# Performance work log

Measured on AMD Instinct MI355X. Metric: run time of the kernel, lower is better.

The kernel has to match this reference:

```python
import jax, jax.numpy as jnp
import numpy as np

V_IN = 32000   # input vocab
V_OUT = 32000  # output vocab
H = 512        # hidden size
T = 128        # encoder max length
B = 64         # batch
MAXLEN = 32    # decoder steps
BOS = 2


def gru_cell(x, h, Wih, Whh, bih, bhh):
    # PyTorch GRU gate order: r, z, n
    gi = x @ Wih.T + bih          # (B, 3H)
    gh = h @ Whh.T + bhh          # (B, 3H)
    i_r, i_z, i_n = jnp.split(gi, 3, axis=-1)
    h_r, h_z, h_n = jnp.split(gh, 3, axis=-1)
    r = jax.nn.sigmoid(i_r + h_r)
    z = jax.nn.sigmoid(i_z + h_z)
    n = jnp.tanh(i_n + r * h_n)
    return (1.0 - z) * n + z * h


def setup_inputs() -> dict:
    key = jax.random.key(0)
    ks = jax.random.split(key, 14)
    s = 1.0 / np.sqrt(H)

    def U(k, shape):
        return jax.random.uniform(k, shape, jnp.float32, -s, s)

    tok = jax.random.randint(ks[0], (T, B), 1, V_IN)
    lengths_X = jax.random.randint(ks[1], (B,), 1, T + 1)
    valid = jnp.arange(T)[:, None] < lengths_X[None, :]
    batch_X = jnp.where(valid, tok, 0)  # PAD=0 beyond length

    return {
        "batch_X": batch_X,
        "lengths_X": lengths_X,
        "max_length": MAXLEN,
        "emb_enc": U(ks[2], (V_IN, H)).at[0].set(0.0),   # padding_idx=0
        "Wih_e": U(ks[3], (3 * H, H)),
        "Whh_e": U(ks[4], (3 * H, H)),
        "bih_e": U(ks[5], (3 * H,)),
        "bhh_e": U(ks[6], (3 * H,)),
        "emb_dec": U(ks[7], (V_OUT, H)).at[0].set(0.0),  # padding_idx=0
        "Wih_d": U(ks[8], (3 * H, H)),
        "Whh_d": U(ks[9], (3 * H, H)),
        "bih_d": U(ks[10], (3 * H,)),
        "bhh_d": U(ks[11], (3 * H,)),
        "Wout": U(ks[12], (V_OUT, H)),
        "bout": U(ks[13], (V_OUT,)),
    }


def reference(batch_X, lengths_X, max_length,
              emb_enc, Wih_e, Whh_e, bih_e, bhh_e,
              emb_dec, Wih_d, Whh_d, bih_d, bhh_d,
              Wout, bout):
    t_len, bsz = batch_X.shape
    emb = emb_enc[batch_X]                               # (T, B, H)
    mask = jnp.arange(t_len)[:, None] < lengths_X[None, :]  # (T, B)

    def enc_step(h, inp):
        x, m = inp
        h_new = gru_cell(x, h, Wih_e, Whh_e, bih_e, bhh_e)
        # packed-sequence semantics: hidden freezes after each seq's length
        return jnp.where(m[:, None], h_new, h), None

    h0 = jnp.zeros((bsz, emb_enc.shape[1]), emb.dtype)
    h_enc, _ = jax.lax.scan(enc_step, h0, (emb, mask))

    def dec_step(carry, _):
        tok, h = carry
        e = emb_dec[tok]                                 # (B, H)
        h = gru_cell(e, h, Wih_d, Whh_d, bih_d, bhh_d)
        logits = h @ Wout.T + bout                       # (B, V_OUT)
        return (jnp.argmax(logits, axis=-1), h), logits

    init = (jnp.full((bsz,), BOS, dtype=batch_X.dtype), h_enc)
    _, outputs = jax.lax.scan(dec_step, init, None, length=max_length)
    return outputs  # (max_length, B, V_OUT)
```

## Files before the change

### kernel.cpp

```cpp
#include <hip/hip_runtime.h>
#include <math.h>

constexpr int NB  = 64;
constexpr int NH  = 512;
constexpr int BOSTOK = 2;

__device__ __forceinline__ float sigmoidf_(float x) { return 1.0f / (1.0f + expf(-x)); }

__global__ __launch_bounds__(256) void k_init(float* __restrict__ eT,
                                              const float* __restrict__ emb_dec) {
    int i = blockIdx.x * 256 + threadIdx.x;
    if (i < NH * NB) eT[i] = emb_dec[BOSTOK * NH + (i >> 6)];
}

__global__ __launch_bounds__(256) void k_xg(const int* __restrict__ tokens,
                                            const float* __restrict__ emb,
                                            float* __restrict__ xg, int total_f4) {
    int idx = blockIdx.x * 256 + threadIdx.x;
    int stride = gridDim.x * 256;
    for (int f = idx; f < total_f4; f += stride) {
        const int tb = f >> 7;
        const int kq = f & 127;
        const int row = tokens[tb];
        ((float4*)xg)[f] = ((const float4*)(emb + (size_t)row * NH))[kq];
    }
}

__global__ __launch_bounds__(256) void k_wpack(const float* __restrict__ Whh,
                                               float4* __restrict__ Wp) {
    const int gk = blockIdx.x;
    const int g = gk >> 7, kq = gk & 127;
    for (int j = threadIdx.x; j < NH; j += 256) {
        const float* src = Whh + ((size_t)(g * NH + j)) * NH + 4 * kq;
        Wp[(size_t)gk * NH + j] = make_float4(src[0], src[1], src[2], src[3]);
    }
}

__global__ __launch_bounds__(256) void k_gi(const float* __restrict__ xg,
                                            const float* __restrict__ Wih,
                                            float* __restrict__ gi) {
    __shared__ __align__(16) float At[2][16][68];
    __shared__ __align__(16) float Bs[2][16][132];
    const int tid  = threadIdx.x;
    const int tb0  = blockIdx.y * 64;
    const int gj0  = blockIdx.x * 128;
    const int g_tb = tid >> 4;
    const int g_gj = tid & 15;
    const int a_tb = tid >> 2, a_kq = tid & 3;
    const int b_gj = tid >> 2, b_kq = tid & 3;

    float4 ra, rb0, rb1;
    ra  = *(const float4*)(xg  + (size_t)(tb0 + a_tb) * NH + 4 * a_kq);
    rb0 = *(const float4*)(Wih + (size_t)(gj0 + b_gj) * NH + 4 * b_kq);
    rb1 = *(const float4*)(Wih + (size_t)(gj0 + b_gj + 64) * NH + 4 * b_kq);

    float acc[4][8];
#pragma unroll
    for (int a = 0; a < 4; ++a)
#pragma unroll
        for (int b = 0; b < 8; ++b) acc[a][b] = 0.f;

    for (int c = 0; c < NH / 16; ++c) {
        const int buf = c & 1;
#pragma unroll
        for (int q = 0; q < 4; ++q) {
            At[buf][4 * a_kq + q][a_tb]      = ((const float*)&ra)[q];
            Bs[buf][4 * b_kq + q][b_gj]      = ((const float*)&rb0)[q];
            Bs[buf][4 * b_kq + q][b_gj + 64] = ((const float*)&rb1)[q];
        }
        __syncthreads();
        if (c + 1 < NH / 16) {
            const int k0 = (c + 1) * 16;
            ra  = *(const float4*)(xg  + (size_t)(tb0 + a_tb) * NH + k0 + 4 * a_kq);
            rb0 = *(const float4*)(Wih + (size_t)(gj0 + b_gj) * NH + k0 + 4 * b_kq);
            rb1 = *(const float4*)(Wih + (size_t)(gj0 + b_gj + 64) * NH + k0 + 4 * b_kq);
        }
#pragma unroll
        for (int k = 0; k < 16; ++k) {
            const float4 av = *(const float4*)&At[buf][k][4 * g_tb];
            const float4 b0 = *(const float4*)&Bs[buf][k][8 * g_gj];
            const float4 b1 = *(const float4*)&Bs[buf][k][8 * g_gj + 4];
            const float* ap  = (const float*)&av;
            const float* bp0 = (const float*)&b0;
            const float* bp1 = (const float*)&b1;
#pragma unroll
            for (int a = 0; a < 4; ++a) {
#pragma unroll
                for (int b = 0; b < 4; ++b) {
                    acc[a][b]     += ap[a] * bp0[b];
                    acc[a][b + 4] += ap[a] * bp1[b];
                }
            }
        }
    }
    float* go = gi + (size_t)tb0 * (3 * NH) + gj0;
#pragma unroll
    for (int a = 0; a < 4; ++a) {
        float4 s0 = make_float4(acc[a][0], acc[a][1], acc[a][2], acc[a][3]);
        float4 s1 = make_float4(acc[a][4], acc[a][5], acc[a][6], acc[a][7]);
        float* r = go + (size_t)(4 * g_tb + a) * (3 * NH) + 8 * g_gj;
        *(float4*)(r)     = s0;
        *(float4*)(r + 4) = s1;
    }
}

__global__ __launch_bounds__(512, 1) void k_enc_recur(
        const float* __restrict__ gi,
        const float4* __restrict__ Wp,
        const float* __restrict__ bih, const float* __restrict__ bhh,
        const int* __restrict__ lengths,
        float* __restrict__ hfin) {
    __shared__ __align__(16) float hbuf[2][NH];
    const int b = blockIdx.x;
    const int j = threadIdx.x;
    const int len = lengths[b];
    const float bir  = bih[j],          bhr = bhh[j];
    const float biz  = bih[NH + j],     bhz = bhh[NH + j];
    const float bin_ = bih[2 * NH + j], bhn = bhh[2 * NH + j];
    hbuf[0][j] = 0.f;
    __syncthreads();
    int cur = 0;
    for (int t = 0; t < len; ++t) {
        const float* __restrict__ hs = hbuf[cur];
        const float* __restrict__ gp = gi + ((size_t)t * NB + b) * (3 * NH);
        float ar = 0.f, az = 0.f, an = 0.f;
#pragma unroll 4
        for (int kq = 0; kq < NH / 4; ++kq) {
            const float4 hq = *(const float4*)&hs[4 * kq];
            const float4 wr = Wp[(size_t)(0 * 128 + kq) * NH + j];
            const float4 wz = Wp[(size_t)(1 * 128 + kq) * NH + j];
            const float4 wn = Wp[(size_t)(2 * 128 + kq) * NH + j];
            ar += wr.x * hq.x + wr.y * hq.y + wr.z * hq.z + wr.w * hq.w;
            az += wz.x * hq.x + wz.y * hq.y + wz.z * hq.z + wz.w * hq.w;
            an += wn.x * hq.x + wn.y * hq.y + wn.z * hq.z + wn.w * hq.w;
        }
        const float r = sigmoidf_(gp[j] + bir + ar + bhr);
        const float z = sigmoidf_(gp[NH + j] + biz + az + bhz);
        const float n = tanhf(gp[2 * NH + j] + bin_ + r * (an + bhn));
        const float hv = (1.f - z) * n + z * hs[j];
        hbuf[cur ^ 1][j] = hv;
        __syncthreads();
        cur ^= 1;
    }
    hfin[(size_t)j * NB + b] = hbuf[cur][j];
}

__global__ __launch_bounds__(256) void k_dec_gru(const float* __restrict__ hc,
                                                 float* __restrict__ hn,
                                                 const float* __restrict__ eT,
                                                 const float* __restrict__ Wih,
                                                 const float* __restrict__ Whh,
                                                 const float* __restrict__ bih,
                                                 const float* __restrict__ bhh) {
    const int tid = threadIdx.x;
    const int b = tid & 63;
    const int jj = tid >> 6;
    const int j = blockIdx.x * 4 + jj;
    const float* __restrict__ ir_w = Wih + (size_t)j * NH;
    const float* __restrict__ iz_w = Wih + (size_t)(NH + j) * NH;
    const float* __restrict__ in_w = Wih + (size_t)(2 * NH + j) * NH;
    const float* __restrict__ hr_w = Whh + (size_t)j * NH;
    const float* __restrict__ hz_w = Whh + (size_t)(NH + j) * NH;
    const float* __restrict__ hn_w = Whh + (size_t)(2 * NH + j) * NH;
    float air = 0.f, aiz = 0.f, ain = 0.f;
    float ahr = 0.f, ahz = 0.f, ahn = 0.f;
#pragma unroll 2
    for (int k = 0; k < NH; k += 4) {
        const float4 a4 = *(const float4*)(ir_w + k);
        const float4 b4 = *(const float4*)(iz_w + k);
        const float4 c4 = *(const float4*)(in_w + k);
        const float4 d4 = *(const float4*)(hr_w + k);
        const float4 e4 = *(const float4*)(hz_w + k);
        const float4 f4 = *(const float4*)(hn_w + k);
        const float e0 = eT[(k + 0) * NB + b];
        const float e1 = eT[(k + 1) * NB + b];
        const float e2 = eT[(k + 2) * NB + b];
        const float e3 = eT[(k + 3) * NB + b];
        const float h0 = hc[(k + 0) * NB + b];
        const float h1 = hc[(k + 1) * NB + b];
        const float h2 = hc[(k + 2) * NB + b];
        const float h3 = hc[(k + 3) * NB + b];
        air += a4.x * e0 + a4.y * e1 + a4.z * e2 + a4.w * e3;
        aiz += b4.x * e0 + b4.y * e1 + b4.z * e2 + b4.w * e3;
        ain += c4.x * e0 + c4.y * e1 + c4.z * e2 + c4.w * e3;
        ahr += d4.x * h0 + d4.y * h1 + d4.z * h2 + d4.w * h3;
        ahz += e4.x * h0 + e4.y * h1 + e4.z * h2 + e4.w * h3;
        ahn += f4.x * h0 + f4.y * h1 + f4.z * h2 + f4.w * h3;
    }
    const float hj = hc[j * NB + b];
    const float r = sigmoidf_(air + bih[j] + ahr + bhh[j]);
    const float z = sigmoidf_(aiz + bih[NH + j] + ahz + bhh[NH + j]);
    const float n = tanhf(ain + bih[2 * NH + j] + r * (ahn + bhh[2 * NH + j]));
    const float hv = (1.f - z) * n + z * hj;
    hn[j * NB + b] = hv;
}

__global__ __launch_bounds__(256) void k_logits(const float* __restrict__ hT,
                                                const float* __restrict__ Wout,
                                                const float* __restrict__ bout,
                                                float* __restrict__ outp, int V) {
    __shared__ __align__(16) float Ws[2][32][128];
    __shared__ __align__(16) float Hs[2][32][64];
    const int tid = threadIdx.x;
    const int v0 = blockIdx.x * 128;
    const int vg = tid & 31;
    const int bg = tid >> 5;
    const int w_vl = tid >> 3;
    const int w_kq = tid & 7;

    float4 rw[4], rh[2];
#pragma unroll
    for (int p = 0; p < 4; ++p)
        rw[p] = *(const float4*)(Wout + (size_t)(v0 + w_vl + 32 * p) * NH + 4 * w_kq);
#pragma unroll
    for (int p = 0; p < 2; ++p)
        rh[p] = ((const float4*)hT)[p * 256 + tid];

    float acc[8][4];
#pragma unroll
    for (int i = 0; i < 8; ++i)
#pragma unroll
        for (int jv = 0; jv < 4; ++jv) acc[i][jv] = 0.f;

    for (int c = 0; c < 16; ++c) {
        const int buf = c & 1;
#pragma unroll
        for (int p = 0; p < 4; ++p)
#pragma unroll
            for (int q = 0; q < 4; ++q)
                Ws[buf][4 * w_kq + q][w_vl + 32 * p] = ((const float*)&rw[p])[q];
#pragma unroll
        for (int p = 0; p < 2; ++p)
            ((float4*)Hs[buf])[p * 256 + tid] = rh[p];
        __syncthreads();
        if (c + 1 < 16) {
            const int k0 = (c + 1) * 32;
#pragma unroll
            for (int p = 0; p < 4; ++p)
                rw[p] = *(const float4*)(Wout + (size_t)(v0 + w_vl + 32 * p) * NH + k0 + 4 * w_kq);
#pragma unroll
            for (int p = 0; p < 2; ++p)
                rh[p] = ((const float4*)(hT + (size_t)k0 * NB))[p * 256 + tid];
        }
#pragma unroll
        for (int k = 0; k < 32; ++k) {
            const float4 w  = *(const float4*)&Ws[buf][k][4 * vg];
            const float4 h0 = *(const float4*)&Hs[buf][k][8 * bg];
            const float4 h1 = *(const float4*)&Hs[buf][k][8 * bg + 4];
            const float* hp0 = (const float*)&h0;
            const float* hp1 = (const float*)&h1;
#pragma unroll
            for (int i = 0; i < 4; ++i) {
                acc[i][0] += hp0[i] * w.x; acc[i][1] += hp0[i] * w.y;
                acc[i][2] += hp0[i] * w.z; acc[i][3] += hp0[i] * w.w;
                acc[i + 4][0] += hp1[i] * w.x; acc[i + 4][1] += hp1[i] * w.y;
                acc[i + 4][2] += hp1[i] * w.z; acc[i + 4][3] += hp1[i] * w.w;
            }
        }
    }
    const float4 bo = *(const float4*)(bout + v0 + 4 * vg);
#pragma unroll
    for (int i = 0; i < 8; ++i) {
        float4 s = make_float4(acc[i][0] + bo.x, acc[i][1] + bo.y,
                               acc[i][2] + bo.z, acc[i][3] + bo.w);
        *(float4*)(outp + (size_t)(8 * bg + i) * V + v0 + 4 * vg) = s;
    }
}

__global__ __launch_bounds__(256) void k_argmax_embed(const float* __restrict__ logits_t,
                                                      const float* __restrict__ emb_dec,
                                                      float* __restrict__ eT,
                                                      int V) {
    const int b = blockIdx.x;
    const int tid = threadIdx.x;
    const float* __restrict__ lp = logits_t + (size_t)b * V;
    float best = -INFINITY;
    int bi = 0x7fffffff;
    for (int v = tid; v < V; v += 256) {
        const float x = lp[v];
        if (x > best) { best = x; bi = v; }
    }
    __shared__ float sv[256];
    __shared__ int si[256];
    sv[tid] = best;
    si[tid] = bi;
    __syncthreads();
    for (int s = 128; s > 0; s >>= 1) {
        if (tid < s) {
            const float ov = sv[tid + s];
            const int oi = si[tid + s];
            if (ov > sv[tid] || (ov == sv[tid] && oi < si[tid])) { sv[tid] = ov; si[tid] = oi; }
        }
        __syncthreads();
    }
    const int tok = si[0];
    const float* __restrict__ er = emb_dec + (size_t)tok * NH;
    for (int k = tid; k < NH; k += 256)
        eT[k * NB + b] = er[k];
}

extern "C" void kernel_launch(void* const* d_in, const int* in_sizes, int n_in,
                              void* d_out, int out_size, void* d_ws, size_t ws_size,
                              hipStream_t stream) {
    const int*   batch_X = (const int*)d_in[0];
    const int*   lengths = (const int*)d_in[1];
    const float* emb_enc = (const float*)d_in[3];
    const float* Wih_e   = (const float*)d_in[4];
    const float* Whh_e   = (const float*)d_in[5];
    const float* bih_e   = (const float*)d_in[6];
    const float* bhh_e   = (const float*)d_in[7];
    const float* emb_dec = (const float*)d_in[8];
    const float* Wih_d   = (const float*)d_in[9];
    const float* Whh_d   = (const float*)d_in[10];
    const float* bih_d   = (const float*)d_in[11];
    const float* bhh_d   = (const float*)d_in[12];
    const float* Wout    = (const float*)d_in[13];
    const float* bout    = (const float*)d_in[14];

    const int T = in_sizes[0] / NB;
    const int V = in_sizes[14];
    const int STEPS = out_size / (NB * V);

    float* out = (float*)d_out;

    float* dh0 = (float*)d_ws;
    float* dh1 = dh0 + NH * NB;
    float* eT  = dh1 + NH * NB;

    const size_t xg_off = (size_t)out_size - (size_t)T * NB * NH;
    const size_t gi_off = xg_off - (size_t)T * NB * 3 * NH;
    const size_t wp_off = gi_off - (size_t)3 * NH * NH;
    const size_t hf_off = wp_off - (size_t)NH * NB;
    float*  xg   = out + xg_off;
    float*  gi   = out + gi_off;
    float4* Wp   = (float4*)(out + wp_off);
    float*  hfin = out + hf_off;

    k_init<<<dim3(NH * NB / 256), dim3(256), 0, stream>>>(eT, emb_dec);
    k_xg<<<dim3(1024), dim3(256), 0, stream>>>(batch_X, emb_enc, xg, T * NB * NH / 4);
    k_wpack<<<dim3(3 * NH / 4), dim3(256), 0, stream>>>(Whh_e, Wp);
    k_gi<<<dim3(3 * NH / 128, T), dim3(256), 0, stream>>>(xg, Wih_e, gi);
    k_enc_recur<<<dim3(NB), dim3(512), 0, stream>>>(gi, Wp, bih_e, bhh_e, lengths, hfin);

    const float* hc = hfin;
    for (int s = 0; s < STEPS; ++s) {
        float* hn = (s & 1) ? dh1 : dh0;
        k_dec_gru<<<dim3(NH / 4), dim3(256), 0, stream>>>(
            hc, hn, eT, Wih_d, Whh_d, bih_d, bhh_d);
        float* out_t = out + (size_t)s * NB * V;
        k_logits<<<dim3(V / 128), dim3(256), 0, stream>>>(hn, Wout, bout, out_t, V);
        if (s + 1 < STEPS)
            k_argmax_embed<<<dim3(NB), dim3(256), 0, stream>>>(out_t, emb_dec, eT, V);
        hc = hn;
    }
}
```

Before: 7.372 ms.

## Split encoder GRU recurrence across 128 blocks with register-resident weights and atomic barriers

The encoder recurrence used to run one block per batch row, and each block streamed the whole packed Whh matrix from memory at every timestep. Now 128 blocks each own 32 hidden units for 8 batch rows. Each block keeps its Whh slice in registers, reduces partial dot products across lanes with DPP row sums, and exchanges hidden state through global memory. Steps are synchronised with per-batch-group atomic counters, which removes the Whh repack kernel and the repeated weight traffic but adds a cross-block spin barrier each step and relies on relaxed atomics for ordering. A minor readfirstlane hint is also added in the decoder GRU kernel.

```diff
diff --git a/kernel.cpp b/kernel.cpp
--- a/kernel.cpp
+++ b/kernel.cpp
@@ -4,13 +4,26 @@
 constexpr int NB  = 64;
 constexpr int NH  = 512;
 constexpr int BOSTOK = 2;
+constexpr int JT = 16;
+constexpr int BT = 8;
 
 __device__ __forceinline__ float sigmoidf_(float x) { return 1.0f / (1.0f + expf(-x)); }
 
+__device__ __forceinline__ float rowsum16(float v) {
+    int x;
+    x = __builtin_amdgcn_mov_dpp(__float_as_int(v), 0x128, 0xf, 0xf, false); v += __int_as_float(x);
+    x = __builtin_amdgcn_mov_dpp(__float_as_int(v), 0x124, 0xf, 0xf, false); v += __int_as_float(x);
+    x = __builtin_amdgcn_mov_dpp(__float_as_int(v), 0x122, 0xf, 0xf, false); v += __int_as_float(x);
+    x = __builtin_amdgcn_mov_dpp(__float_as_int(v), 0x121, 0xf, 0xf, false); v += __int_as_float(x);
+    return v;
+}
+
 __global__ __launch_bounds__(256) void k_init(float* __restrict__ eT,
-                                              const float* __restrict__ emb_dec) {
+                                              const float* __restrict__ emb_dec,
+                                              int* __restrict__ bar) {
     int i = blockIdx.x * 256 + threadIdx.x;
     if (i < NH * NB) eT[i] = emb_dec[BOSTOK * NH + (i >> 6)];
+    if (i < BT) __hip_atomic_store(&bar[i], 0, __ATOMIC_RELAXED, __HIP_MEMORY_SCOPE_AGENT);
 }
 
 __global__ __launch_bounds__(256) void k_xg(const int* __restrict__ tokens,
@@ -23,16 +36,6 @@
         const int kq = f & 127;
         const int row = tokens[tb];
         ((float4*)xg)[f] = ((const float4*)(emb + (size_t)row * NH))[kq];
-    }
-}
-
-__global__ __launch_bounds__(256) void k_wpack(const float* __restrict__ Whh,
-                                               float4* __restrict__ Wp) {
-    const int gk = blockIdx.x;
-    const int g = gk >> 7, kq = gk & 127;
-    for (int j = threadIdx.x; j < NH; j += 256) {
-        const float* src = Whh + ((size_t)(g * NH + j)) * NH + 4 * kq;
-        Wp[(size_t)gk * NH + j] = make_float4(src[0], src[1], src[2], src[3]);
     }
 }
 
@@ -104,45 +107,127 @@
     }
 }
 
-__global__ __launch_bounds__(512, 1) void k_enc_recur(
+__global__ __launch_bounds__(256, 1) void k_enc_recur(
         const float* __restrict__ gi,
-        const float4* __restrict__ Wp,
+        const float* __restrict__ Whh,
         const float* __restrict__ bih, const float* __restrict__ bhh,
         const int* __restrict__ lengths,
-        float* __restrict__ hfin) {
-    __shared__ __align__(16) float hbuf[2][NH];
-    const int b = blockIdx.x;
-    const int j = threadIdx.x;
-    const int len = lengths[b];
-    const float bir  = bih[j],          bhr = bhh[j];
-    const float biz  = bih[NH + j],     bhz = bhh[NH + j];
-    const float bin_ = bih[2 * NH + j], bhn = bhh[2 * NH + j];
-    hbuf[0][j] = 0.f;
-    __syncthreads();
-    int cur = 0;
-    for (int t = 0; t < len; ++t) {
-        const float* __restrict__ hs = hbuf[cur];
-        const float* __restrict__ gp = gi + ((size_t)t * NB + b) * (3 * NH);
-        float ar = 0.f, az = 0.f, an = 0.f;
-#pragma unroll 4
-        for (int kq = 0; kq < NH / 4; ++kq) {
-            const float4 hq = *(const float4*)&hs[4 * kq];
-            const float4 wr = Wp[(size_t)(0 * 128 + kq) * NH + j];
-            const float4 wz = Wp[(size_t)(1 * 128 + kq) * NH + j];
-            const float4 wn = Wp[(size_t)(2 * 128 + kq) * NH + j];
-            ar += wr.x * hq.x + wr.y * hq.y + wr.z * hq.z + wr.w * hq.w;
-            az += wz.x * hq.x + wz.y * hq.y + wz.z * hq.z + wz.w * hq.w;
-            an += wn.x * hq.x + wn.y * hq.y + wn.z * hq.z + wn.w * hq.w;
-        }
-        const float r = sigmoidf_(gp[j] + bir + ar + bhr);
-        const float z = sigmoidf_(gp[NH + j] + biz + az + bhz);
-        const float n = tanhf(gp[2 * NH + j] + bin_ + r * (an + bhn));
-        const float hv = (1.f - z) * n + z * hs[j];
-        hbuf[cur ^ 1][j] = hv;
-        __syncthreads();
-        cur ^= 1;
-    }
-    hfin[(size_t)j * NB + b] = hbuf[cur][j];
+        float* __restrict__ hx,
+        int* __restrict__ bar,
+        float* __restrict__ hfin,
+        int T) {
+    __shared__ __align__(16) float4 hsh[8 * 128];
+    const int tid = threadIdx.x;
+    const int jt = blockIdx.x >> 3;
+    const int bt = blockIdx.x & 7;
+    const int j0 = jt * 32;
+    const int b0 = bt * 8;
+    const int jg = tid >> 4;
+    const int ks = tid & 15;
+    const int k0 = ks * 32;
+
+    const int jo = j0 + jg * 2 + (ks >> 3);
+    const int bo = b0 + (ks & 7);
+
+    float4 wv[6][8];
+#pragma unroll
+    for (int jl = 0; jl < 2; ++jl)
+#pragma unroll
+        for (int g = 0; g < 3; ++g) {
+            const float* wr = Whh + ((size_t)(g * NH + j0 + jg * 2 + jl)) * NH + k0;
+#pragma unroll
+            for (int q = 0; q < 8; ++q)
+                wv[jl * 3 + g][q] = *(const float4*)(wr + 4 * q);
+        }
+
+    const float bir = bih[jo], biz = bih[NH + jo], bin_ = bih[2 * NH + jo];
+    const float bhr = bhh[jo], bhz = bhh[NH + jo], bhn  = bhh[2 * NH + jo];
+    const int   len = lengths[bo];
+    const float* __restrict__ gpr = gi + (size_t)bo * (3 * NH) + jo;
+    float hlast = 0.f;
+
+    for (int t = 0; t < T; ++t) {
+        if (t > 0 && tid == 0) {
+            const int tgt = JT * t;
+            while (__hip_atomic_load(&bar[bt], __ATOMIC_RELAXED, __HIP_MEMORY_SCOPE_AGENT) < tgt)
+                __builtin_amdgcn_s_sleep(1);
+        }
+        __syncthreads();
+
+        if (t == 0) {
+#pragma unroll
+            for (int i = 0; i < 4; ++i)
+                hsh[tid + i * 256] = make_float4(0.f, 0.f, 0.f, 0.f);
+        } else {
+            float4 v[4];
+#pragma unroll
+            for (int i = 0; i < 4; ++i) {
+                const int P = tid + i * 256;
+                const int bl = P >> 7, p = P & 127;
+                const int q = p ^ ((p >> 3) & 7);
+                float* src = hx + (size_t)(b0 + bl) * NH + q * 4;
+                v[i].x = __hip_atomic_load(src + 0, __ATOMIC_RELAXED, __HIP_MEMORY_SCOPE_AGENT);
+                v[i].y = __hip_atomic_load(src + 1, __ATOMIC_RELAXED, __HIP_MEMORY_SCOPE_AGENT);
+                v[i].z = __hip_atomic_load(src + 2, __ATOMIC_RELAXED, __HIP_MEMORY_SCOPE_AGENT);
+                v[i].w = __hip_atomic_load(src + 3, __ATOMIC_RELAXED, __HIP_MEMORY_SCOPE_AGENT);
+            }
+#pragma unroll
+            for (int i = 0; i < 4; ++i) {
+                const int P = tid + i * 256;
+                hsh[(P >> 7) * 128 + (P & 127)] = v[i];
+            }
+        }
+        __syncthreads();
+
+        float sr = 0.f, sz = 0.f, sn = 0.f;
+#pragma unroll
+        for (int b = 0; b < 8; ++b) {
+            float4 hq[8];
+#pragma unroll
+            for (int kk = 0; kk < 8; ++kk) {
+                const int q = ks * 8 + kk;
+                hq[kk] = hsh[b * 128 + (q ^ (ks & 7))];
+            }
+            float pr0 = 0.f, pz0 = 0.f, pn0 = 0.f, pr1 = 0.f, pz1 = 0.f, pn1 = 0.f;
+#pragma unroll
+            for (int kk = 0; kk < 8; ++kk) {
+                const float4 h4 = hq[kk];
+                const float4 w0 = wv[0][kk], w1 = wv[1][kk], w2 = wv[2][kk];
+                const float4 w3 = wv[3][kk], w4 = wv[4][kk], w5 = wv[5][kk];
+                pr0 += w0.x * h4.x + w0.y * h4.y + w0.z * h4.z + w0.w * h4.w;
+                pz0 += w1.x * h4.x + w1.y * h4.y + w1.z * h4.z + w1.w * h4.w;
+                pn0 += w2.x * h4.x + w2.y * h4.y + w2.z * h4.z + w2.w * h4.w;
+                pr1 += w3.x * h4.x + w3.y * h4.y + w3.z * h4.z + w3.w * h4.w;
+                pz1 += w4.x * h4.x + w4.y * h4.y + w4.z * h4.z + w4.w * h4.w;
+                pn1 += w5.x * h4.x + w5.y * h4.y + w5.z * h4.z + w5.w * h4.w;
+            }
+            pr0 = rowsum16(pr0); pz0 = rowsum16(pz0); pn0 = rowsum16(pn0);
+            pr1 = rowsum16(pr1); pz1 = rowsum16(pz1); pn1 = rowsum16(pn1);
+            if ((ks & 7) == b) {
+                if (ks >> 3) { sr = pr1; sz = pz1; sn = pn1; }
+                else         { sr = pr0; sz = pz0; sn = pn0; }
+            }
+        }
+
+        const float* __restrict__ gp = gpr + (size_t)t * NB * (3 * NH);
+        const float gr = gp[0], gz = gp[NH], gn = gp[2 * NH];
+        const int qj = jo >> 2;
+        const int pj = qj ^ ((qj >> 3) & 7);
+        const float hold = ((const float*)&hsh[(ks & 7) * 128 + pj])[jo & 3];
+        const float r = sigmoidf_(gr + bir + sr + bhr);
+        const float z = sigmoidf_(gz + biz + sz + bhz);
+        const float n = tanhf(gn + bin_ + r * (sn + bhn));
+        const float hv = (1.f - z) * n + z * hold;
+        if (t < len) {
+            __hip_atomic_store(hx + (size_t)bo * NH + jo, hv,
+                               __ATOMIC_RELAXED, __HIP_MEMORY_SCOPE_AGENT);
+            hlast = hv;
+        }
+        __syncthreads();
+        if (tid == 0)
+            __hip_atomic_fetch_add(&bar[bt], 1, __ATOMIC_RELAXED, __HIP_MEMORY_SCOPE_AGENT);
+    }
+    hfin[(size_t)jo * NB + bo] = hlast;
 }
 
 __global__ __launch_bounds__(256) void k_dec_gru(const float* __restrict__ hc,
@@ -154,7 +239,7 @@
                                                  const float* __restrict__ bhh) {
     const int tid = threadIdx.x;
     const int b = tid & 63;
-    const int jj = tid >> 6;
+    const int jj = __builtin_amdgcn_readfirstlane(tid >> 6);
     const int j = blockIdx.x * 4 + jj;
     const float* __restrict__ ir_w = Wih + (size_t)j * NH;
     const float* __restrict__ iz_w = Wih + (size_t)(NH + j) * NH;
@@ -326,21 +411,21 @@
     float* dh0 = (float*)d_ws;
     float* dh1 = dh0 + NH * NB;
     float* eT  = dh1 + NH * NB;
+    int*   bar = (int*)(eT + NH * NB);
+    float* hx  = dh0;
 
     const size_t xg_off = (size_t)out_size - (size_t)T * NB * NH;
     const size_t gi_off = xg_off - (size_t)T * NB * 3 * NH;
-    const size_t wp_off = gi_off - (size_t)3 * NH * NH;
-    const size_t hf_off = wp_off - (size_t)NH * NB;
-    float*  xg   = out + xg_off;
-    float*  gi   = out + gi_off;
-    float4* Wp   = (float4*)(out + wp_off);
-    float*  hfin = out + hf_off;
-
-    k_init<<<dim3(NH * NB / 256), dim3(256), 0, stream>>>(eT, emb_dec);
+    const size_t hf_off = gi_off - (size_t)NH * NB;
+    float* xg   = out + xg_off;
+    float* gi   = out + gi_off;
+    float* hfin = out + hf_off;
+
+    k_init<<<dim3(NH * NB / 256), dim3(256), 0, stream>>>(eT, emb_dec, bar);
     k_xg<<<dim3(1024), dim3(256), 0, stream>>>(batch_X, emb_enc, xg, T * NB * NH / 4);
-    k_wpack<<<dim3(3 * NH / 4), dim3(256), 0, stream>>>(Whh_e, Wp);
     k_gi<<<dim3(3 * NH / 128, T), dim3(256), 0, stream>>>(xg, Wih_e, gi);
-    k_enc_recur<<<dim3(NB), dim3(512), 0, stream>>>(gi, Wp, bih_e, bhh_e, lengths, hfin);
+    k_enc_recur<<<dim3(JT * BT), dim3(256), 0, stream>>>(
+        gi, Whh_e, bih_e, bhh_e, lengths, hx, bar, hfin, T);
 
     const float* hc = hfin;
     for (int s = 0; s < STEPS; ++s) {
```

Measured after the change: 5.928 ms. -19.6%, faster.
